# Optimization experiments

Measured on AMD Instinct MI355X. Metric: run time of the kernel, lower is better.

Reference implementation:

```python
import jax, jax.numpy as jnp
import numpy as np

N = 100000   # nodes
E = 500000   # edges
D = 128      # embed_dim
DEPTH = 2
EPS = 1e-5   # BatchNorm1d eps


def setup_inputs() -> dict:
    key = jax.random.key(0)
    ks = jax.random.split(key, 5)
    x = jax.random.normal(ks[0], (N, D), dtype=jnp.float32)
    edge_index = jax.random.randint(ks[1], (2, E), 0, N)
    edge_weight = jax.random.uniform(ks[2], (E,), dtype=jnp.float32)
    # per-layer params: nn.Linear weight [out,in] for both the plain linear and GCNConv lin
    lin_w = jax.random.normal(ks[3], (DEPTH, D, D), dtype=jnp.float32) * 0.05
    gcn_w = jax.random.normal(ks[4], (DEPTH, D, D), dtype=jnp.float32) * 0.05
    gamma = jnp.ones((DEPTH, D), dtype=jnp.float32)
    beta = jnp.zeros((DEPTH, D), dtype=jnp.float32)
    return {"x": x, "edge_index": edge_index, "edge_weight": edge_weight,
            "lin_w": lin_w, "gcn_w": gcn_w, "gamma": gamma, "beta": beta}


def reference(x, edge_index, edge_weight, lin_w, gcn_w, gamma, beta):
    row, col = edge_index[0], edge_index[1]  # source, target (flow source_to_target)
    # PyG gcn_norm with add_self_loops=False
    deg = jax.ops.segment_sum(edge_weight, col, num_segments=N)
    deg_safe = jnp.where(deg > 0, deg, 1.0)
    dinv = jnp.where(deg > 0, jax.lax.rsqrt(deg_safe), 0.0)  # deg^{-1/2}, 0 for isolated
    norm = dinv[row] * edge_weight * dinv[col]                # [E]

    h = x
    for i in range(DEPTH):
        hl = h @ lin_w[i].T                                   # plain linear branch
        hg = h @ gcn_w[i].T                                   # GCNConv lin
        agg = jax.ops.segment_sum(norm[:, None] * hg[row], col, num_segments=N)
        h = hl + agg
        # BatchNorm1d (training mode: batch statistics, biased var)
        mean = h.mean(axis=0)
        var = h.var(axis=0)
        h = (h - mean) * jax.lax.rsqrt(var + EPS) * gamma[i] + beta[i]
        if i != DEPTH - 1:
            h = jax.nn.relu(h)
    return h
```

## Files before the change

kernel.cpp:

```cpp
#include <hip/hip_runtime.h>
#include <hip/hip_bf16.h>

#define NN 100000
#define EE 500000
#define DD 128
#define NDEPTH 2
#define EPSV 1e-5f
#define NCHUNK 1024
#define NBLK ((NN + NCHUNK - 1) / NCHUNK)
#define NPB 2000
#define RPB 50

typedef __attribute__((ext_vector_type(4))) float f32x4;
typedef __attribute__((ext_vector_type(4))) int i32x4;
typedef __attribute__((ext_vector_type(2))) unsigned int u32x2;
typedef __attribute__((ext_vector_type(8))) short bf16x8;
typedef __attribute__((ext_vector_type(4))) short bf16x4;

static __device__ __forceinline__ short f2bf(float x) {
  union { float f; unsigned u; } v; v.f = x;
  unsigned r = v.u + 0x7fffu + ((v.u >> 16) & 1u);
  return (short)(r >> 16);
}
static __device__ __forceinline__ float bfbits2f(unsigned hi16) {
  union { unsigned u; float f; } v; v.u = hi16;
  return v.f;
}

__global__ void k_convert_w(const float* __restrict__ lw, const float* __restrict__ gw,
                            short* __restrict__ wbf) {
  int i = blockIdx.x * 256 + threadIdx.x;
  if (i < NDEPTH * DD * DD) {
    wbf[i] = f2bf(lw[i]);
    wbf[NDEPTH * DD * DD + i] = f2bf(gw[i]);
  }
}

__global__ void k_edge1(const int* __restrict__ ei, const float* __restrict__ ew,
                        unsigned long long* __restrict__ dc) {
  int e = blockIdx.x * 256 + threadIdx.x;
  if (e < EE) {
    int c = ei[EE + e];
    unsigned long long pack = (1ULL << 44) |
        (unsigned long long)(ew[e] * 4294967296.0f + 0.5f);
    atomicAdd(dc + c, pack);
  }
}

__global__ void k_dinv(const unsigned long long* __restrict__ dc,
                       float* __restrict__ dinv, int* __restrict__ cnt) {
  int i = blockIdx.x * 256 + threadIdx.x;
  if (i < NN) {
    unsigned long long v = dc[i];
    cnt[i] = (int)(v >> 44);
    float deg = (float)(v & ((1ULL << 44) - 1)) * (1.0f / 4294967296.0f);
    dinv[i] = deg > 0.f ? rsqrtf(deg) : 0.f;
  }
}

__global__ __launch_bounds__(256) void k_scan_part(const int* __restrict__ cnt,
                                                   int* __restrict__ part) {
  int b = blockIdx.x, t = threadIdx.x, lane = t & 63, wid = t >> 6;
  int base = b * NCHUNK + t * 4;
  int s = 0;
  if (base + 3 < NN) {
    i32x4 v = *(const i32x4*)(cnt + base);
    s = v[0] + v[1] + v[2] + v[3];
  } else {
    for (int j = 0; j < 4; ++j) if (base + j < NN) s += cnt[base + j];
  }
  for (int d = 32; d > 0; d >>= 1) s += __shfl_down(s, d);
  __shared__ int wsum[4];
  if (lane == 0) wsum[wid] = s;
  __syncthreads();
  if (t == 0) part[b] = wsum[0] + wsum[1] + wsum[2] + wsum[3];
}

__global__ void k_scan_mid(int* __restrict__ part, int* __restrict__ rowptr) {
  __shared__ int sm[128];
  int t = threadIdx.x;
  int v = (t < NBLK) ? part[t] : 0;
  sm[t] = v;
  __syncthreads();
  for (int off = 1; off < 128; off <<= 1) {
    int a = sm[t];
    int b = (t >= off) ? sm[t - off] : 0;
    __syncthreads();
    sm[t] = a + b;
    __syncthreads();
  }
  if (t < NBLK) part[t] = (t == 0) ? 0 : sm[t - 1];
  if (t == 127) rowptr[NN] = sm[127];
}

__global__ __launch_bounds__(256) void k_scan_final(const int* __restrict__ cnt,
    const int* __restrict__ part, int* __restrict__ rowptr, int* __restrict__ cursor) {
  int b = blockIdx.x, t = threadIdx.x, lane = t & 63, wid = t >> 6;
  int base = b * NCHUNK + t * 4;
  int c0 = 0, c1 = 0, c2 = 0, c3 = 0;
  if (base + 3 < NN) {
    i32x4 v = *(const i32x4*)(cnt + base);
    c0 = v[0]; c1 = v[1]; c2 = v[2]; c3 = v[3];
  } else {
    if (base < NN) c0 = cnt[base];
    if (base + 1 < NN) c1 = cnt[base + 1];
    if (base + 2 < NN) c2 = cnt[base + 2];
    if (base + 3 < NN) c3 = cnt[base + 3];
  }
  int s = c0 + c1 + c2 + c3;
  int v = s;
  for (int d = 1; d < 64; d <<= 1) {
    int u = __shfl_up(v, d);
    if (lane >= d) v += u;
  }
  __shared__ int wsum[4];
  if (lane == 63) wsum[wid] = v;
  __syncthreads();
  int woff = 0;
  for (int w = 0; w < wid; ++w) woff += wsum[w];
  int excl = part[b] + woff + (v - s);
  if (base < NN)     { rowptr[base]     = excl; cursor[base]     = excl; excl += c0; }
  if (base + 1 < NN) { rowptr[base + 1] = excl; cursor[base + 1] = excl; excl += c1; }
  if (base + 2 < NN) { rowptr[base + 2] = excl; cursor[base + 2] = excl; excl += c2; }
  if (base + 3 < NN) { rowptr[base + 3] = excl; cursor[base + 3] = excl; }
}

__global__ void k_edge2(const int* __restrict__ ei, const float* __restrict__ ew,
                        const float* __restrict__ dinv, int* __restrict__ cursor,
                        int* __restrict__ srow, float* __restrict__ snorm) {
  int e = blockIdx.x * 256 + threadIdx.x;
  if (e < EE) {
    int r = ei[e], c = ei[EE + e];
    float nrm = dinv[r] * ew[e] * dinv[c];
    int pos = atomicAdd(cursor + c, 1);
    srow[pos] = r;
    snorm[pos] = nrm;
  }
}

template<int APPLY>
__global__ __launch_bounds__(512) void k_dualgemm(const void* __restrict__ Hv,
    const short* __restrict__ Wl, const short* __restrict__ Wg,
    const float* __restrict__ sb, unsigned short* __restrict__ tmpo,
    unsigned short* __restrict__ hg) {
  __shared__ short lw[2 * DD * DD];
  int tid = threadIdx.x;

#pragma unroll
  for (int c = 0; c < 8; ++c) {
    int q = c * 512 + tid;
    int region = q >> 11;
    int row = (q >> 4) & 127;
    int u = q & 15;
    const short* src = (region ? Wg : Wl) + row * DD + ((u ^ (row & 7)) * 8);
    *(bf16x8*)(lw + q * 8) = *(const bf16x8*)src;
  }

  int lane = tid & 63, wv = tid >> 6;
  int row0 = blockIdx.x * 128 + wv * 16;
  int m = lane & 15, g = lane >> 4;

  bf16x8 hb[4];
  if (row0 < NN) {
#pragma unroll
    for (int s = 0; s < 4; ++s) {
      float f[8];
      if (APPLY) {
        const unsigned short* H = (const unsigned short*)Hv;
        bf16x8 hv = *(const bf16x8*)(H + (size_t)(row0 + m) * DD + s * 32 + g * 8);
#pragma unroll
        for (int k2 = 0; k2 < 8; ++k2)
          f[k2] = bfbits2f(((unsigned)(unsigned short)hv[k2]) << 16);
      } else {
        const float* H = (const float*)Hv;
        f32x4 v0 = *(const f32x4*)(H + (size_t)(row0 + m) * DD + s * 32 + g * 8);
        f32x4 v1 = *(const f32x4*)(H + (size_t)(row0 + m) * DD + s * 32 + g * 8 + 4);
#pragma unroll
        for (int k2 = 0; k2 < 4; ++k2) { f[k2] = v0[k2]; f[k2 + 4] = v1[k2]; }
      }
      if (APPLY) {
        f32x4 sc0 = *(const f32x4*)(sb + s * 32 + g * 8);
        f32x4 sc1 = *(const f32x4*)(sb + s * 32 + g * 8 + 4);
        f32x4 bi0 = *(const f32x4*)(sb + DD + s * 32 + g * 8);
        f32x4 bi1 = *(const f32x4*)(sb + DD + s * 32 + g * 8 + 4);
#pragma unroll
        for (int k2 = 0; k2 < 4; ++k2) {
          f[k2]     = fmaxf(f[k2]     * sc0[k2] + bi0[k2], 0.f);
          f[k2 + 4] = fmaxf(f[k2 + 4] * sc1[k2] + bi1[k2], 0.f);
        }
      }
      bf16x8 tt;
#pragma unroll
      for (int k2 = 0; k2 < 8; ++k2) tt[k2] = f2bf(f[k2]);
      hb[s] = tt;
    }
  }

  __syncthreads();
  if (row0 >= NN) return;

  int mx = m & 7;
#pragma unroll
  for (int t = 0; t < 8; ++t) {
    f32x4 accl; accl[0] = 0.f; accl[1] = 0.f; accl[2] = 0.f; accl[3] = 0.f;
    f32x4 accg = accl;
#pragma unroll
    for (int s = 0; s < 4; ++s) {
      int u = (s * 4 + g) ^ mx;
      int base = (t * 16 + m) * DD + u * 8;
      bf16x8 wlf = *(const bf16x8*)(lw + base);
      bf16x8 wgf = *(const bf16x8*)(lw + DD * DD + base);
      accl = __builtin_amdgcn_mfma_f32_16x16x32_bf16(wlf, hb[s], accl, 0, 0, 0);
      accg = __builtin_amdgcn_mfma_f32_16x16x32_bf16(wgf, hb[s], accg, 0, 0, 0);
    }
    size_t r = (size_t)(row0 + m);
    bf16x4 l4, h4;
    l4[0] = f2bf(accl[0]); l4[1] = f2bf(accl[1]); l4[2] = f2bf(accl[2]); l4[3] = f2bf(accl[3]);
    h4[0] = f2bf(accg[0]); h4[1] = f2bf(accg[1]); h4[2] = f2bf(accg[2]); h4[3] = f2bf(accg[3]);
    *(bf16x4*)(tmpo + r * DD + t * 16 + g * 4) = l4;
    *(bf16x4*)(hg + r * DD + t * 16 + g * 4) = h4;
  }
}

__global__ __launch_bounds__(256) void k_agg(const int* __restrict__ rowptr,
    const int* __restrict__ srow, const float* __restrict__ snorm,
    const unsigned int* __restrict__ hgu, unsigned int* __restrict__ tmpu) {
  int node = (blockIdx.x * 256 + (int)threadIdx.x) >> 6;
  int lane = threadIdx.x & 63;
  if (node >= NN) return;
  node = __builtin_amdgcn_readfirstlane(node);
  int beg = rowptr[node], end = rowptr[node + 1];
  float ax = 0.f, ay = 0.f;
  int j = beg;
  for (; j + 3 < end; j += 4) {
    int r0 = srow[j], r1 = srow[j + 1], r2 = srow[j + 2], r3 = srow[j + 3];
    float w0 = snorm[j], w1 = snorm[j + 1], w2 = snorm[j + 2], w3 = snorm[j + 3];
    unsigned u0 = hgu[r0 * 64 + lane];
    unsigned u1 = hgu[r1 * 64 + lane];
    unsigned u2 = hgu[r2 * 64 + lane];
    unsigned u3 = hgu[r3 * 64 + lane];
    ax += w0 * bfbits2f(u0 << 16) + w1 * bfbits2f(u1 << 16)
        + w2 * bfbits2f(u2 << 16) + w3 * bfbits2f(u3 << 16);
    ay += w0 * bfbits2f(u0 & 0xffff0000u) + w1 * bfbits2f(u1 & 0xffff0000u)
        + w2 * bfbits2f(u2 & 0xffff0000u) + w3 * bfbits2f(u3 & 0xffff0000u);
  }
  for (; j < end; ++j) {
    int r = srow[j];
    float w = snorm[j];
    unsigned u = hgu[r * 64 + lane];
    ax += w * bfbits2f(u << 16);
    ay += w * bfbits2f(u & 0xffff0000u);
  }
  unsigned* tp = tmpu + (size_t)node * 64 + lane;
  unsigned hl = *tp;
  float t0 = bfbits2f(hl << 16) + ax;
  float t1 = bfbits2f(hl & 0xffff0000u) + ay;
  unsigned p0 = (unsigned)(unsigned short)f2bf(t0);
  unsigned p1 = (unsigned)(unsigned short)f2bf(t1);
  *tp = p0 | (p1 << 16);
}

__global__ __launch_bounds__(256) void k_bnstats(const unsigned int* __restrict__ h,
    float* __restrict__ psum, float* __restrict__ pss) {
  int b = blockIdx.x, t = threadIdx.x;
  int cg = t & 31, rs = t >> 5;
  f32x4 s; s[0] = 0.f; s[1] = 0.f; s[2] = 0.f; s[3] = 0.f;
  f32x4 q = s;
  int r0 = b * RPB;
  for (int r = r0 + rs; r < r0 + RPB; r += 8) {
    u32x2 u = *(const u32x2*)(h + (size_t)r * 64 + cg * 2);
    f32x4 v;
    v[0] = bfbits2f(u[0] << 16); v[1] = bfbits2f(u[0] & 0xffff0000u);
    v[2] = bfbits2f(u[1] << 16); v[3] = bfbits2f(u[1] & 0xffff0000u);
    s += v; q += v * v;
  }
  __shared__ f32x4 ls[8][32], lq[8][32];
  ls[rs][cg] = s; lq[rs][cg] = q;
  __syncthreads();
  if (t < 32) {
    f32x4 a = ls[0][t], qq = lq[0][t];
#pragma unroll
    for (int k = 1; k < 8; ++k) { a += ls[k][t]; qq += lq[k][t]; }
#pragma unroll
    for (int c = 0; c < 4; ++c) {
      psum[(t * 4 + c) * NPB + b] = a[c];
      pss [(t * 4 + c) * NPB + b] = qq[c];
    }
  }
}

__global__ __launch_bounds__(256) void k_bnreduce(const float* __restrict__ psum,
    const float* __restrict__ pss, const float* __restrict__ gamma,
    const float* __restrict__ beta, float* __restrict__ sb) {
  int col = blockIdx.x, t = threadIdx.x;
  float s = 0.f, q = 0.f;
  for (int i = t; i < NPB; i += 256) { s += psum[col * NPB + i]; q += pss[col * NPB + i]; }
  for (int d = 32; d > 0; d >>= 1) { s += __shfl_down(s, d); q += __shfl_down(q, d); }
  __shared__ float lws[4], lwq[4];
  int wid = t >> 6, lane = t & 63;
  if (lane == 0) { lws[wid] = s; lwq[wid] = q; }
  __syncthreads();
  if (t == 0) {
    float S = lws[0] + lws[1] + lws[2] + lws[3];
    float Q = lwq[0] + lwq[1] + lwq[2] + lwq[3];
    float mean = S * (1.f / NN);
    float var = Q * (1.f / NN) - mean * mean;
    float sc = rsqrtf(var + EPSV) * gamma[col];
    sb[col] = sc;
    sb[DD + col] = beta[col] - mean * sc;
  }
}

__global__ void k_bnapply(const unsigned int* __restrict__ hb, const float* __restrict__ sb,
                          float* __restrict__ out) {
  int i = blockIdx.x * 256 + threadIdx.x;
  if (i >= NN * DD / 4) return;
  int d0 = (i * 4) & (DD - 1);
  u32x2 u = *(const u32x2*)(hb + i * 2);
  f32x4 o;
  o[0] = bfbits2f(u[0] << 16)          * sb[d0]     + sb[DD + d0];
  o[1] = bfbits2f(u[0] & 0xffff0000u)  * sb[d0 + 1] + sb[DD + d0 + 1];
  o[2] = bfbits2f(u[1] << 16)          * sb[d0 + 2] + sb[DD + d0 + 2];
  o[3] = bfbits2f(u[1] & 0xffff0000u)  * sb[d0 + 3] + sb[DD + d0 + 3];
  ((f32x4*)out)[i] = o;
}

extern "C" void kernel_launch(void* const* d_in, const int* in_sizes, int n_in,
                              void* d_out, int out_size, void* d_ws, size_t ws_size,
                              hipStream_t stream) {
  const float* x     = (const float*)d_in[0];
  const int*   ei    = (const int*)d_in[1];
  const float* ew    = (const float*)d_in[2];
  const float* lin_w = (const float*)d_in[3];
  const float* gcn_w = (const float*)d_in[4];
  const float* gamma = (const float*)d_in[5];
  const float* beta  = (const float*)d_in[6];
  float* out = (float*)d_out;

  char* ws = (char*)d_ws;
  size_t off = 0;
  auto alloc = [&](size_t bytes) -> void* {
    void* p = ws + off;
    off += (bytes + 255) & ~(size_t)255;
    return p;
  };
  unsigned short* hg   = (unsigned short*)alloc((size_t)NN * DD * 2);
  unsigned short* tmpb = (unsigned short*)alloc((size_t)NN * DD * 2);
  float* snorm  = (float*)alloc((size_t)EE * 4);
  int*   srow   = (int*)alloc((size_t)EE * 4);
  unsigned long long* dc = (unsigned long long*)alloc((size_t)NN * 8);
  float* dinv   = (float*)alloc((size_t)NN * 4);
  int*   rowptr = (int*)alloc((size_t)(NN + 1) * 4);
  int*   cursor = (int*)alloc((size_t)NN * 4);
  int*   cnt    = (int*)alloc((size_t)NN * 4);
  int*   part   = (int*)alloc((size_t)NBLK * 4);
  short* wbf    = (short*)alloc((size_t)2 * NDEPTH * DD * DD * 2);
  float* psum   = (float*)alloc((size_t)DD * NPB * 4);
  float* pss    = (float*)alloc((size_t)DD * NPB * 4);
  float* sb     = (float*)alloc((size_t)2 * DD * 4);

  hipMemsetAsync(dc, 0, (size_t)NN * 8, stream);

  k_convert_w<<<(NDEPTH * DD * DD + 255) / 256, 256, 0, stream>>>(lin_w, gcn_w, wbf);
  k_edge1<<<(EE + 255) / 256, 256, 0, stream>>>(ei, ew, dc);
  k_dinv<<<(NN + 255) / 256, 256, 0, stream>>>(dc, dinv, cnt);
  k_scan_part<<<NBLK, 256, 0, stream>>>(cnt, part);
  k_scan_mid<<<1, 128, 0, stream>>>(part, rowptr);
  k_scan_final<<<NBLK, 256, 0, stream>>>(cnt, part, rowptr, cursor);
  k_edge2<<<(EE + 255) / 256, 256, 0, stream>>>(ei, ew, dinv, cursor, srow, snorm);

  const short* Wl0 = wbf;
  const short* Wg0 = wbf + (size_t)NDEPTH * DD * DD;
  const short* Wl1 = wbf + (size_t)DD * DD;
  const short* Wg1 = wbf + (size_t)NDEPTH * DD * DD + (size_t)DD * DD;
  const int GEMMBLK = (NN + 127) / 128;

  k_dualgemm<0><<<GEMMBLK, 512, 0, stream>>>(x, Wl0, Wg0, sb, tmpb, hg);
  k_agg<<<(NN + 3) / 4, 256, 0, stream>>>(rowptr, srow, snorm, (const unsigned int*)hg,
                                          (unsigned int*)tmpb);
  k_bnstats<<<NPB, 256, 0, stream>>>((const unsigned int*)tmpb, psum, pss);
  k_bnreduce<<<DD, 256, 0, stream>>>(psum, pss, gamma, beta, sb);

  k_dualgemm<1><<<GEMMBLK, 512, 0, stream>>>(tmpb, Wl1, Wg1, sb, tmpb, hg);
  k_agg<<<(NN + 3) / 4, 256, 0, stream>>>(rowptr, srow, snorm, (const unsigned int*)hg,
                                          (unsigned int*)tmpb);
  k_bnstats<<<NPB, 256, 0, stream>>>((const unsigned int*)tmpb, psum, pss);
  k_bnreduce<<<DD, 256, 0, stream>>>(psum, pss, gamma + DD, beta + DD, sb);
  k_bnapply<<<(NN * DD / 4 + 255) / 256, 256, 0, stream>>>((const unsigned int*)tmpb, sb, out);
}
```

Baseline: 242.4 us.

## Factor GCN normalization into GEMM and aggregation; pack edge records

The symmetric normalization dinv[row]*w*dinv[col] is no longer computed per edge. The source-side dinv is folded into the GCN GEMM output scaling, and the target-side dinv is applied once per node after aggregation. Edge source index and raw weight are packed into one int2 record, so the aggregation loop issues one 8-byte load per edge instead of two separate ones, and k_edge2 skips two dinv gathers. This changes rounding slightly, because the bf16 hg now carries the dinv scaling before quantization.

```diff
diff --git a/kernel.cpp b/kernel.cpp
--- a/kernel.cpp
+++ b/kernel.cpp
@@ -126,23 +126,23 @@
 }
 
 __global__ void k_edge2(const int* __restrict__ ei, const float* __restrict__ ew,
-                        const float* __restrict__ dinv, int* __restrict__ cursor,
-                        int* __restrict__ srow, float* __restrict__ snorm) {
+                        int* __restrict__ cursor, int2* __restrict__ eb) {
   int e = blockIdx.x * 256 + threadIdx.x;
   if (e < EE) {
     int r = ei[e], c = ei[EE + e];
-    float nrm = dinv[r] * ew[e] * dinv[c];
     int pos = atomicAdd(cursor + c, 1);
-    srow[pos] = r;
-    snorm[pos] = nrm;
+    int2 rec;
+    rec.x = r;
+    rec.y = __float_as_int(ew[e]);
+    eb[pos] = rec;
   }
 }
 
 template<int APPLY>
 __global__ __launch_bounds__(512) void k_dualgemm(const void* __restrict__ Hv,
     const short* __restrict__ Wl, const short* __restrict__ Wg,
-    const float* __restrict__ sb, unsigned short* __restrict__ tmpo,
-    unsigned short* __restrict__ hg) {
+    const float* __restrict__ sb, const float* __restrict__ dinvp,
+    unsigned short* __restrict__ tmpo, unsigned short* __restrict__ hg) {
   __shared__ short lw[2 * DD * DD];
   int tid = threadIdx.x;
 
@@ -161,7 +161,9 @@
   int m = lane & 15, g = lane >> 4;
 
   bf16x8 hb[4];
+  float dv = 0.f;
   if (row0 < NN) {
+    dv = dinvp[row0 + m];
 #pragma unroll
     for (int s = 0; s < 4; ++s) {
       float f[8];
@@ -216,14 +218,15 @@
     size_t r = (size_t)(row0 + m);
     bf16x4 l4, h4;
     l4[0] = f2bf(accl[0]); l4[1] = f2bf(accl[1]); l4[2] = f2bf(accl[2]); l4[3] = f2bf(accl[3]);
-    h4[0] = f2bf(accg[0]); h4[1] = f2bf(accg[1]); h4[2] = f2bf(accg[2]); h4[3] = f2bf(accg[3]);
+    h4[0] = f2bf(accg[0] * dv); h4[1] = f2bf(accg[1] * dv);
+    h4[2] = f2bf(accg[2] * dv); h4[3] = f2bf(accg[3] * dv);
     *(bf16x4*)(tmpo + r * DD + t * 16 + g * 4) = l4;
     *(bf16x4*)(hg + r * DD + t * 16 + g * 4) = h4;
   }
 }
 
 __global__ __launch_bounds__(256) void k_agg(const int* __restrict__ rowptr,
-    const int* __restrict__ srow, const float* __restrict__ snorm,
+    const int2* __restrict__ eb, const float* __restrict__ dinv,
     const unsigned int* __restrict__ hgu, unsigned int* __restrict__ tmpu) {
   int node = (blockIdx.x * 256 + (int)threadIdx.x) >> 6;
   int lane = threadIdx.x & 63;
@@ -233,24 +236,27 @@
   float ax = 0.f, ay = 0.f;
   int j = beg;
   for (; j + 3 < end; j += 4) {
-    int r0 = srow[j], r1 = srow[j + 1], r2 = srow[j + 2], r3 = srow[j + 3];
-    float w0 = snorm[j], w1 = snorm[j + 1], w2 = snorm[j + 2], w3 = snorm[j + 3];
-    unsigned u0 = hgu[r0 * 64 + lane];
-    unsigned u1 = hgu[r1 * 64 + lane];
-    unsigned u2 = hgu[r2 * 64 + lane];
-    unsigned u3 = hgu[r3 * 64 + lane];
+    int2 e0 = eb[j], e1 = eb[j + 1], e2 = eb[j + 2], e3 = eb[j + 3];
+    unsigned u0 = hgu[e0.x * 64 + lane];
+    unsigned u1 = hgu[e1.x * 64 + lane];
+    unsigned u2 = hgu[e2.x * 64 + lane];
+    unsigned u3 = hgu[e3.x * 64 + lane];
+    float w0 = __int_as_float(e0.y), w1 = __int_as_float(e1.y);
+    float w2 = __int_as_float(e2.y), w3 = __int_as_float(e3.y);
     ax += w0 * bfbits2f(u0 << 16) + w1 * bfbits2f(u1 << 16)
         + w2 * bfbits2f(u2 << 16) + w3 * bfbits2f(u3 << 16);
     ay += w0 * bfbits2f(u0 & 0xffff0000u) + w1 * bfbits2f(u1 & 0xffff0000u)
         + w2 * bfbits2f(u2 & 0xffff0000u) + w3 * bfbits2f(u3 & 0xffff0000u);
   }
   for (; j < end; ++j) {
-    int r = srow[j];
-    float w = snorm[j];
-    unsigned u = hgu[r * 64 + lane];
+    int2 e0 = eb[j];
+    float w = __int_as_float(e0.y);
+    unsigned u = hgu[e0.x * 64 + lane];
     ax += w * bfbits2f(u << 16);
     ay += w * bfbits2f(u & 0xffff0000u);
   }
+  float dvn = dinv[node];
+  ax *= dvn; ay *= dvn;
   unsigned* tp = tmpu + (size_t)node * 64 + lane;
   unsigned hl = *tp;
   float t0 = bfbits2f(hl << 16) + ax;
@@ -346,8 +352,7 @@
   };
   unsigned short* hg   = (unsigned short*)alloc((size_t)NN * DD * 2);
   unsigned short* tmpb = (unsigned short*)alloc((size_t)NN * DD * 2);
-  float* snorm  = (float*)alloc((size_t)EE * 4);
-  int*   srow   = (int*)alloc((size_t)EE * 4);
+  int2*  eb     = (int2*)alloc((size_t)EE * 8);
   unsigned long long* dc = (unsigned long long*)alloc((size_t)NN * 8);
   float* dinv   = (float*)alloc((size_t)NN * 4);
   int*   rowptr = (int*)alloc((size_t)(NN + 1) * 4);
@@ -367,7 +372,7 @@
   k_scan_part<<<NBLK, 256, 0, stream>>>(cnt, part);
   k_scan_mid<<<1, 128, 0, stream>>>(part, rowptr);
   k_scan_final<<<NBLK, 256, 0, stream>>>(cnt, part, rowptr, cursor);
-  k_edge2<<<(EE + 255) / 256, 256, 0, stream>>>(ei, ew, dinv, cursor, srow, snorm);
+  k_edge2<<<(EE + 255) / 256, 256, 0, stream>>>(ei, ew, cursor, eb);
 
   const short* Wl0 = wbf;
   const short* Wg0 = wbf + (size_t)NDEPTH * DD * DD;
@@ -375,14 +380,14 @@
   const short* Wg1 = wbf + (size_t)NDEPTH * DD * DD + (size_t)DD * DD;
   const int GEMMBLK = (NN + 127) / 128;
 
-  k_dualgemm<0><<<GEMMBLK, 512, 0, stream>>>(x, Wl0, Wg0, sb, tmpb, hg);
-  k_agg<<<(NN + 3) / 4, 256, 0, stream>>>(rowptr, srow, snorm, (const unsigned int*)hg,
+  k_dualgemm<0><<<GEMMBLK, 512, 0, stream>>>(x, Wl0, Wg0, sb, dinv, tmpb, hg);
+  k_agg<<<(NN + 3) / 4, 256, 0, stream>>>(rowptr, eb, dinv, (const unsigned int*)hg,
                                           (unsigned int*)tmpb);
   k_bnstats<<<NPB, 256, 0, stream>>>((const unsigned int*)tmpb, psum, pss);
   k_bnreduce<<<DD, 256, 0, stream>>>(psum, pss, gamma, beta, sb);
 
-  k_dualgemm<1><<<GEMMBLK, 512, 0, stream>>>(tmpb, Wl1, Wg1, sb, tmpb, hg);
-  k_agg<<<(NN + 3) / 4, 256, 0, stream>>>(rowptr, srow, snorm, (const unsigned int*)hg,
+  k_dualgemm<1><<<GEMMBLK, 512, 0, stream>>>(tmpb, Wl1, Wg1, sb, dinv, tmpb, hg);
+  k_agg<<<(NN + 3) / 4, 256, 0, stream>>>(rowptr, eb, dinv, (const unsigned int*)hg,
                                           (unsigned int*)tmpb);
   k_bnstats<<<NPB, 256, 0, stream>>>((const unsigned int*)tmpb, psum, pss);
   k_bnreduce<<<DD, 256, 0, stream>>>(psum, pss, gamma + DD, beta + DD, sb);
```

After: 237.9 us. About the same (-1.9%).
